# Kernel tuning notes

Measured on AMD Instinct MI355X. Metric: run time of the kernel, lower is better.

The kernel has to match this reference:

```python
import jax, jax.numpy as jnp
import numpy as np


def setup_inputs() -> dict:
    key = jax.random.key(0)
    k0, k1, k2, k3, k4 = jax.random.split(key, 5)
    T, B, S = 256, 8, 256          # tgt_len, batch, src_len
    QD, KD, VD = 512, 512, 512     # query_dim, key_dim, value_dim
    query = jax.random.normal(k0, (T, B, QD), dtype=jnp.float32)
    keys = jax.random.normal(k1, (B, S, KD), dtype=jnp.float32)
    values = jax.random.normal(k2, (B, S, VD), dtype=jnp.float32)
    # torch nn.Linear weights: (out_features, in_features)
    Wa = jax.random.normal(k3, (KD, QD + KD), dtype=jnp.float32) * 0.02
    va = jax.random.normal(k4, (1, KD), dtype=jnp.float32) * 0.02
    return {"query": query, "keys": keys, "values": values, "Wa": Wa, "va": va}


def reference(query, keys, values, Wa, va):
    # Wa(cat([q, k])) == q @ Wa[:, :QD].T + k @ Wa[:, QD:].T (algebraic split,
    # same math as the original concat, avoids materializing the concat tensor).
    QD = query.shape[-1]
    Wq, Wk = Wa[:, :QD], Wa[:, QD:]                      # (KD,QD), (KD,KD)
    qp = jnp.einsum('tbq,kq->btk', query, Wq)             # (B,T,KD)
    kp = jnp.einsum('bsk,hk->bsh', keys, Wk)              # (B,S,KD)
    hidden = jnp.tanh(qp[:, :, None, :] + kp[:, None, :, :])  # (B,T,S,KD)
    weight = jnp.einsum('btsk,k->bts', hidden, va[0])     # (B,T,S)
    score = jax.nn.softmax(weight, axis=-1)               # softmax over src
    ctx = jnp.einsum('bts,bsv->btv', score, values)       # (B,T,VD)
    return (score, ctx)
```

## Files before the change

### kernel.cpp

```cpp
#include <hip/hip_runtime.h>
#include <hip/hip_bf16.h>

#define TT   256
#define BB   8
#define SS   256
#define DD   512
#define C2LOG2E 2.8853900817779268f
#define LOG2E   1.4426950408889634f

typedef __attribute__((ext_vector_type(8))) short bf16x8;
typedef __attribute__((ext_vector_type(4))) float f32x4;

__device__ __forceinline__ unsigned short f2bf(float f) {
    unsigned u = __builtin_bit_cast(unsigned, f);
    u += 0x7FFFu + ((u >> 16) & 1u);
    return (unsigned short)(u >> 16);
}
__device__ __forceinline__ float bf2f(unsigned short h) {
    unsigned u = (unsigned)h << 16;
    return __builtin_bit_cast(float, u);
}

#define LDK 72
__global__ __launch_bounds__(256) void gemm_mfma(const float* __restrict__ query,
                                                 const float* __restrict__ keys,
                                                 const float* __restrict__ Wa,
                                                 float* __restrict__ eq,
                                                 float* __restrict__ ekT) {
    __shared__ __align__(16) unsigned char smem[4 * 64 * LDK * 2];
    unsigned short* sAh = (unsigned short*)smem;
    unsigned short* sAl = sAh + 64 * LDK;
    unsigned short* sBh = sAl + 64 * LDK;
    unsigned short* sBl = sBh + 64 * LDK;
    float* Cst = (float*)smem;

    const int idx = blockIdx.x;
    const int b   = idx & 7;
    const int r2  = idx >> 3;
    const int q   = r2 & 3;
    const int x   = (r2 >> 2) & 7;
    const int z   = r2 >> 5;
    const bool isQ = (z == 0);

    const float* A  = isQ ? query : keys;
    const int strideR = isQ ? BB * DD : DD;
    const int strideB = isQ ? DD : SS * DD;
    const float* Bsrc = Wa + (isQ ? 0 : DD);

    const int tileN = x * 64;

    const int tid = threadIdx.x;
    const int rb  = tid >> 4;
    const int c4  = tid & 15;

    const float* arow0 = A + (size_t)b * strideB + (size_t)(q * 64) * strideR;
    const float* brow0 = Bsrc + (size_t)tileN * (2 * DD);

    float4 av[4], bv[4];
    #pragma unroll
    for (int i = 0; i < 4; ++i) {
        av[i] = *(const float4*)(arow0 + (size_t)(rb + 16*i) * strideR + c4 * 4);
        bv[i] = *(const float4*)(brow0 + (size_t)(rb + 16*i) * (2*DD) + c4 * 4);
    }

    const int w    = tid >> 6;
    const int lane = tid & 63;
    const int wm   = (w >> 1) * 32;
    const int wn   = (w & 1) * 32;
    const int r16  = lane & 15;
    const int k8   = (lane >> 4) * 8;

    f32x4 acc[2][2] = {};

    for (int kb = 0; kb < DD; kb += 64) {
        __syncthreads();
        #pragma unroll
        for (int i = 0; i < 4; ++i) {
            const int row = rb + 16 * i;
            float4 a = av[i], bq = bv[i];
            ushort4 ah, al, bh, bl;
            ah.x = f2bf(a.x); al.x = f2bf(a.x - bf2f(ah.x));
            ah.y = f2bf(a.y); al.y = f2bf(a.y - bf2f(ah.y));
            ah.z = f2bf(a.z); al.z = f2bf(a.z - bf2f(ah.z));
            ah.w = f2bf(a.w); al.w = f2bf(a.w - bf2f(ah.w));
            bh.x = f2bf(bq.x); bl.x = f2bf(bq.x - bf2f(bh.x));
            bh.y = f2bf(bq.y); bl.y = f2bf(bq.y - bf2f(bh.y));
            bh.z = f2bf(bq.z); bl.z = f2bf(bq.z - bf2f(bh.z));
            bh.w = f2bf(bq.w); bl.w = f2bf(bq.w - bf2f(bh.w));
            *(ushort4*)(sAh + row * LDK + c4 * 4) = ah;
            *(ushort4*)(sAl + row * LDK + c4 * 4) = al;
            *(ushort4*)(sBh + row * LDK + c4 * 4) = bh;
            *(ushort4*)(sBl + row * LDK + c4 * 4) = bl;
        }
        __syncthreads();
        if (kb + 64 < DD) {
            #pragma unroll
            for (int i = 0; i < 4; ++i) {
                av[i] = *(const float4*)(arow0 + (size_t)(rb + 16*i) * strideR + kb + 64 + c4 * 4);
                bv[i] = *(const float4*)(brow0 + (size_t)(rb + 16*i) * (2*DD) + kb + 64 + c4 * 4);
            }
        }
        #pragma unroll
        for (int ks = 0; ks < 2; ++ks) {
            const int ko = ks * 32 + k8;
            bf16x8 a_h[2], a_l[2], b_h[2], b_l[2];
            #pragma unroll
            for (int mt = 0; mt < 2; ++mt) {
                a_h[mt] = *(const bf16x8*)(sAh + (wm + mt*16 + r16) * LDK + ko);
                a_l[mt] = *(const bf16x8*)(sAl + (wm + mt*16 + r16) * LDK + ko);
            }
            #pragma unroll
            for (int nt = 0; nt < 2; ++nt) {
                b_h[nt] = *(const bf16x8*)(sBh + (wn + nt*16 + r16) * LDK + ko);
                b_l[nt] = *(const bf16x8*)(sBl + (wn + nt*16 + r16) * LDK + ko);
            }
            #pragma unroll
            for (int mt = 0; mt < 2; ++mt)
                #pragma unroll
                for (int nt = 0; nt < 2; ++nt) {
                    acc[mt][nt] = __builtin_amdgcn_mfma_f32_16x16x32_bf16(a_h[mt], b_h[nt], acc[mt][nt], 0, 0, 0);
                    acc[mt][nt] = __builtin_amdgcn_mfma_f32_16x16x32_bf16(a_h[mt], b_l[nt], acc[mt][nt], 0, 0, 0);
                    acc[mt][nt] = __builtin_amdgcn_mfma_f32_16x16x32_bf16(a_l[mt], b_h[nt], acc[mt][nt], 0, 0, 0);
                }
        }
    }

    const int crow = (lane >> 4) * 4;
    if (isQ) {
        #pragma unroll
        for (int mt = 0; mt < 2; ++mt)
            #pragma unroll
            for (int nt = 0; nt < 2; ++nt)
                #pragma unroll
                for (int i = 0; i < 4; ++i) {
                    const int m = b * 256 + q * 64 + wm + mt*16 + crow + i;
                    const int n = tileN + wn + nt*16 + r16;
                    eq[(size_t)m * DD + n] = __builtin_amdgcn_exp2f(acc[mt][nt][i] * C2LOG2E);
                }
    } else {
        __syncthreads();
        #pragma unroll
        for (int mt = 0; mt < 2; ++mt)
            #pragma unroll
            for (int nt = 0; nt < 2; ++nt)
                #pragma unroll
                for (int i = 0; i < 4; ++i)
                    Cst[(wm + mt*16 + crow + i) * 69 + wn + nt*16 + r16] =
                        __builtin_amdgcn_exp2f(acc[mt][nt][i] * C2LOG2E);
        __syncthreads();
        const int n  = tid & 63;
        const int sg = tid >> 6;
        float* dst = ekT + (size_t)b * DD * SS + (size_t)(tileN + n) * SS + q * 64 + sg * 16;
        #pragma unroll
        for (int j4 = 0; j4 < 4; ++j4) {
            float4 o;
            o.x = Cst[(sg*16 + j4*4 + 0) * 69 + n];
            o.y = Cst[(sg*16 + j4*4 + 1) * 69 + n];
            o.z = Cst[(sg*16 + j4*4 + 2) * 69 + n];
            o.w = Cst[(sg*16 + j4*4 + 3) * 69 + n];
            *(float4*)(dst + j4 * 4) = o;
        }
    }
}

__global__ __launch_bounds__(1024, 8) void attn_fused(const float* __restrict__ eq,
                                                      const float* __restrict__ ekT,
                                                      const float* __restrict__ va,
                                                      const float* __restrict__ values,
                                                      float* __restrict__ out) {
    __shared__ __align__(16) float eq_s[4][512];
    __shared__ __align__(16) float vb_s[512];
    __shared__ __align__(16) float wacc[4][4][256];
    __shared__ __align__(16) float w_s[4][256];
    __shared__ float red_m[4][4];
    __shared__ float red_s[4][4];

    const int tid  = threadIdx.x;
    const int lane = tid & 63;
    const int w    = tid >> 6;
    const int kq   = w & 3;
    const int sq   = w >> 2;
    const int idx  = blockIdx.x;
    const int b    = idx & 7;
    const int t0   = (idx >> 3) * 4;

    if (tid < 512) {
        const float4* qsrc = (const float4*)(eq + (size_t)(b * TT + t0) * DD);
        ((float4*)&eq_s[0][0])[tid] = qsrc[tid];
    } else if (tid < 640) {
        const int i = tid - 512;
        float4 v = ((const float4*)va)[i];
        ((float4*)vb_s)[i] = make_float4(-2.f*v.x, -2.f*v.y, -2.f*v.z, -2.f*v.w);
    }
    __syncthreads();

    const int kbase = kq * 128;
    const int s     = sq * 64 + lane;
    const float* ekp = ekT + (size_t)b * DD * SS + (size_t)kbase * SS + s;
    const float4* eqr0 = (const float4*)&eq_s[0][kbase];
    const float4* eqr1 = (const float4*)&eq_s[1][kbase];
    const float4* eqr2 = (const float4*)&eq_s[2][kbase];
    const float4* eqr3 = (const float4*)&eq_s[3][kbase];
    const float4* vbr  = (const float4*)&vb_s[kbase];

    float acc0 = 0.f, acc1 = 0.f, acc2 = 0.f, acc3 = 0.f;

    #pragma unroll 4
    for (int kb = 0; kb < 128; kb += 4) {
        float ek0 = ekp[(size_t)(kb + 0) * SS];
        float ek1 = ekp[(size_t)(kb + 1) * SS];
        float ek2 = ekp[(size_t)(kb + 2) * SS];
        float ek3 = ekp[(size_t)(kb + 3) * SS];
        float4 e0 = eqr0[kb >> 2];
        float4 e1 = eqr1[kb >> 2];
        float4 e2 = eqr2[kb >> 2];
        float4 e3 = eqr3[kb >> 2];
        float4 vb = vbr[kb >> 2];
#define ASTEP(EC, EK, VC)                                                      \
        acc0 = fmaf(VC, __builtin_amdgcn_rcpf(fmaf(e0.EC, EK, 1.0f)), acc0);   \
        acc1 = fmaf(VC, __builtin_amdgcn_rcpf(fmaf(e1.EC, EK, 1.0f)), acc1);   \
        acc2 = fmaf(VC, __builtin_amdgcn_rcpf(fmaf(e2.EC, EK, 1.0f)), acc2);   \
        acc3 = fmaf(VC, __builtin_amdgcn_rcpf(fmaf(e3.EC, EK, 1.0f)), acc3);
        ASTEP(x, ek0, vb.x)
        ASTEP(y, ek1, vb.y)
        ASTEP(z, ek2, vb.z)
        ASTEP(w, ek3, vb.w)
#undef ASTEP
    }

    wacc[0][kq][s] = acc0;
    wacc[1][kq][s] = acc1;
    wacc[2][kq][s] = acc2;
    wacc[3][kq][s] = acc3;
    __syncthreads();

    float wt[4], p[4];
    if (kq == 0) {
        #pragma unroll
        for (int t = 0; t < 4; ++t)
            wt[t] = (wacc[t][0][s] + wacc[t][1][s]) + (wacc[t][2][s] + wacc[t][3][s]);
        #pragma unroll
        for (int t = 0; t < 4; ++t) {
            float m = wt[t];
            #pragma unroll
            for (int off = 32; off > 0; off >>= 1) m = fmaxf(m, __shfl_xor(m, off));
            if (lane == 0) red_m[sq][t] = m;
        }
    }
    __syncthreads();
    if (kq == 0) {
        #pragma unroll
        for (int t = 0; t < 4; ++t) {
            float M = fmaxf(fmaxf(red_m[0][t], red_m[1][t]),
                            fmaxf(red_m[2][t], red_m[3][t]));
            p[t] = __builtin_amdgcn_exp2f((wt[t] - M) * LOG2E);
            float sm = p[t];
            #pragma unroll
            for (int off = 32; off > 0; off >>= 1) sm += __shfl_xor(sm, off);
            if (lane == 0) red_s[sq][t] = sm;
        }
    }
    __syncthreads();
    if (kq == 0) {
        #pragma unroll
        for (int t = 0; t < 4; ++t) {
            float inv = __builtin_amdgcn_rcpf((red_s[0][t] + red_s[1][t]) +
                                              (red_s[2][t] + red_s[3][t]));
            float sc = p[t] * inv;
            out[(size_t)(b * TT + t0 + t) * SS + s] = sc;
            w_s[t][s] = sc;
        }
    }
    __syncthreads();

    const int v  = tid & 511;
    const int th = tid >> 9;
    const float* vcol = values + (size_t)b * SS * DD + v;
    const float4* wr0 = (const float4*)&w_s[th * 2][0];
    const float4* wr1 = (const float4*)&w_s[th * 2 + 1][0];
    float c0 = 0.f, c1 = 0.f;
    #pragma unroll 4
    for (int ss = 0; ss < SS; ss += 4) {
        float4 w0 = wr0[ss >> 2];
        float4 w1 = wr1[ss >> 2];
        float v0 = vcol[(size_t)(ss + 0) * DD];
        float v1 = vcol[(size_t)(ss + 1) * DD];
        float v2 = vcol[(size_t)(ss + 2) * DD];
        float v3 = vcol[(size_t)(ss + 3) * DD];
        c0 = fmaf(w0.x, v0, c0); c1 = fmaf(w1.x, v0, c1);
        c0 = fmaf(w0.y, v1, c0); c1 = fmaf(w1.y, v1, c1);
        c0 = fmaf(w0.z, v2, c0); c1 = fmaf(w1.z, v2, c1);
        c0 = fmaf(w0.w, v3, c0); c1 = fmaf(w1.w, v3, c1);
    }
    float* octx = out + (size_t)BB * TT * SS + (size_t)(b * TT + t0 + th * 2) * DD + v;
    octx[0]  = c0;
    octx[DD] = c1;
}

extern "C" void kernel_launch(void* const* d_in, const int* in_sizes, int n_in,
                              void* d_out, int out_size, void* d_ws, size_t ws_size,
                              hipStream_t stream) {
    const float* query  = (const float*)d_in[0];
    const float* keys   = (const float*)d_in[1];
    const float* values = (const float*)d_in[2];
    const float* Wa     = (const float*)d_in[3];
    const float* va     = (const float*)d_in[4];
    float* out = (float*)d_out;

    float* eq  = (float*)d_ws;
    float* ekT = eq + (size_t)BB * TT * DD;

    gemm_mfma<<<512, 256, 0, stream>>>(query, keys, Wa, eq, ekT);
    attn_fused<<<512, 1024, 0, stream>>>(eq, ekT, va, values, out);
}
```

Measured before the change: 71.05 us.

## Combine four reciprocals into one and store projected keys row-major

Groups of four terms v/(1+e_q*e_k) are now summed over a common denominator, so each group needs one rcp instead of four. Projected keys are written row-major, which drops the transpose through shared memory in the GEMM and lets the attention kernel read them with float4 loads. The softmax reduction now spreads its work across all four wave groups instead of only kq==0. The product of four denominators could overflow when the exponentials are large, and each lane's reads of ek are now strided across s rather than coalesced.

```diff
diff --git a/kernel.cpp b/kernel.cpp
--- a/kernel.cpp
+++ b/kernel.cpp
@@ -26,13 +26,12 @@
                                                  const float* __restrict__ keys,
                                                  const float* __restrict__ Wa,
                                                  float* __restrict__ eq,
-                                                 float* __restrict__ ekT) {
+                                                 float* __restrict__ ekR) {
     __shared__ __align__(16) unsigned char smem[4 * 64 * LDK * 2];
     unsigned short* sAh = (unsigned short*)smem;
     unsigned short* sAl = sAh + 64 * LDK;
     unsigned short* sBh = sAl + 64 * LDK;
     unsigned short* sBl = sBh + 64 * LDK;
-    float* Cst = (float*)smem;
 
     const int idx = blockIdx.x;
     const int b   = idx & 7;
@@ -46,9 +45,9 @@
     const int strideR = isQ ? BB * DD : DD;
     const int strideB = isQ ? DD : SS * DD;
     const float* Bsrc = Wa + (isQ ? 0 : DD);
+    float* dst = isQ ? eq : ekR;
 
     const int tileN = x * 64;
-
     const int tid = threadIdx.x;
     const int rb  = tid >> 4;
     const int c4  = tid & 15;
@@ -126,45 +125,20 @@
     }
 
     const int crow = (lane >> 4) * 4;
-    if (isQ) {
-        #pragma unroll
-        for (int mt = 0; mt < 2; ++mt)
-            #pragma unroll
-            for (int nt = 0; nt < 2; ++nt)
-                #pragma unroll
-                for (int i = 0; i < 4; ++i) {
-                    const int m = b * 256 + q * 64 + wm + mt*16 + crow + i;
-                    const int n = tileN + wn + nt*16 + r16;
-                    eq[(size_t)m * DD + n] = __builtin_amdgcn_exp2f(acc[mt][nt][i] * C2LOG2E);
-                }
-    } else {
-        __syncthreads();
-        #pragma unroll
-        for (int mt = 0; mt < 2; ++mt)
-            #pragma unroll
-            for (int nt = 0; nt < 2; ++nt)
-                #pragma unroll
-                for (int i = 0; i < 4; ++i)
-                    Cst[(wm + mt*16 + crow + i) * 69 + wn + nt*16 + r16] =
-                        __builtin_amdgcn_exp2f(acc[mt][nt][i] * C2LOG2E);
-        __syncthreads();
-        const int n  = tid & 63;
-        const int sg = tid >> 6;
-        float* dst = ekT + (size_t)b * DD * SS + (size_t)(tileN + n) * SS + q * 64 + sg * 16;
-        #pragma unroll
-        for (int j4 = 0; j4 < 4; ++j4) {
-            float4 o;
-            o.x = Cst[(sg*16 + j4*4 + 0) * 69 + n];
-            o.y = Cst[(sg*16 + j4*4 + 1) * 69 + n];
-            o.z = Cst[(sg*16 + j4*4 + 2) * 69 + n];
-            o.w = Cst[(sg*16 + j4*4 + 3) * 69 + n];
-            *(float4*)(dst + j4 * 4) = o;
-        }
-    }
+    #pragma unroll
+    for (int mt = 0; mt < 2; ++mt)
+        #pragma unroll
+        for (int nt = 0; nt < 2; ++nt)
+            #pragma unroll
+            for (int i = 0; i < 4; ++i) {
+                const int m = b * 256 + q * 64 + wm + mt*16 + crow + i;
+                const int n = tileN + wn + nt*16 + r16;
+                dst[(size_t)m * DD + n] = __builtin_amdgcn_exp2f(acc[mt][nt][i] * C2LOG2E);
+            }
 }
 
 __global__ __launch_bounds__(1024, 8) void attn_fused(const float* __restrict__ eq,
-                                                      const float* __restrict__ ekT,
+                                                      const float* __restrict__ ekR,
                                                       const float* __restrict__ va,
                                                       const float* __restrict__ values,
                                                       float* __restrict__ out) {
@@ -196,7 +170,7 @@
 
     const int kbase = kq * 128;
     const int s     = sq * 64 + lane;
-    const float* ekp = ekT + (size_t)b * DD * SS + (size_t)kbase * SS + s;
+    const float* ekp = ekR + (size_t)(b * SS + s) * DD + kbase;
     const float4* eqr0 = (const float4*)&eq_s[0][kbase];
     const float4* eqr1 = (const float4*)&eq_s[1][kbase];
     const float4* eqr2 = (const float4*)&eq_s[2][kbase];
@@ -207,25 +181,29 @@
 
     #pragma unroll 4
     for (int kb = 0; kb < 128; kb += 4) {
-        float ek0 = ekp[(size_t)(kb + 0) * SS];
-        float ek1 = ekp[(size_t)(kb + 1) * SS];
-        float ek2 = ekp[(size_t)(kb + 2) * SS];
-        float ek3 = ekp[(size_t)(kb + 3) * SS];
+        float4 ek = *(const float4*)(ekp + kb);
+        float4 vb = vbr[kb >> 2];
         float4 e0 = eqr0[kb >> 2];
         float4 e1 = eqr1[kb >> 2];
         float4 e2 = eqr2[kb >> 2];
         float4 e3 = eqr3[kb >> 2];
-        float4 vb = vbr[kb >> 2];
-#define ASTEP(EC, EK, VC)                                                      \
-        acc0 = fmaf(VC, __builtin_amdgcn_rcpf(fmaf(e0.EC, EK, 1.0f)), acc0);   \
-        acc1 = fmaf(VC, __builtin_amdgcn_rcpf(fmaf(e1.EC, EK, 1.0f)), acc1);   \
-        acc2 = fmaf(VC, __builtin_amdgcn_rcpf(fmaf(e2.EC, EK, 1.0f)), acc2);   \
-        acc3 = fmaf(VC, __builtin_amdgcn_rcpf(fmaf(e3.EC, EK, 1.0f)), acc3);
-        ASTEP(x, ek0, vb.x)
-        ASTEP(y, ek1, vb.y)
-        ASTEP(z, ek2, vb.z)
-        ASTEP(w, ek3, vb.w)
-#undef ASTEP
+#define GSTEP(EQ, ACC)                                                         \
+        {                                                                      \
+            float y0 = fmaf(EQ.x, ek.x, 1.0f);                                 \
+            float y1 = fmaf(EQ.y, ek.y, 1.0f);                                 \
+            float y2 = fmaf(EQ.z, ek.z, 1.0f);                                 \
+            float y3 = fmaf(EQ.w, ek.w, 1.0f);                                 \
+            float d01 = y0 * y1, d23 = y2 * y3;                                \
+            float n01 = fmaf(vb.x, y1, vb.y * y0);                             \
+            float n23 = fmaf(vb.z, y3, vb.w * y2);                             \
+            float num = fmaf(n01, d23, n23 * d01);                             \
+            ACC = fmaf(num, __builtin_amdgcn_rcpf(d01 * d23), ACC);            \
+        }
+        GSTEP(e0, acc0)
+        GSTEP(e1, acc1)
+        GSTEP(e2, acc2)
+        GSTEP(e3, acc3)
+#undef GSTEP
     }
 
     wacc[0][kq][s] = acc0;
@@ -234,42 +212,31 @@
     wacc[3][kq][s] = acc3;
     __syncthreads();
 
-    float wt[4], p[4];
-    if (kq == 0) {
-        #pragma unroll
-        for (int t = 0; t < 4; ++t)
-            wt[t] = (wacc[t][0][s] + wacc[t][1][s]) + (wacc[t][2][s] + wacc[t][3][s]);
-        #pragma unroll
-        for (int t = 0; t < 4; ++t) {
-            float m = wt[t];
-            #pragma unroll
-            for (int off = 32; off > 0; off >>= 1) m = fmaxf(m, __shfl_xor(m, off));
-            if (lane == 0) red_m[sq][t] = m;
-        }
-    }
-    __syncthreads();
-    if (kq == 0) {
-        #pragma unroll
-        for (int t = 0; t < 4; ++t) {
-            float M = fmaxf(fmaxf(red_m[0][t], red_m[1][t]),
-                            fmaxf(red_m[2][t], red_m[3][t]));
-            p[t] = __builtin_amdgcn_exp2f((wt[t] - M) * LOG2E);
-            float sm = p[t];
-            #pragma unroll
-            for (int off = 32; off > 0; off >>= 1) sm += __shfl_xor(sm, off);
-            if (lane == 0) red_s[sq][t] = sm;
-        }
-    }
-    __syncthreads();
-    if (kq == 0) {
-        #pragma unroll
-        for (int t = 0; t < 4; ++t) {
-            float inv = __builtin_amdgcn_rcpf((red_s[0][t] + red_s[1][t]) +
-                                              (red_s[2][t] + red_s[3][t]));
-            float sc = p[t] * inv;
-            out[(size_t)(b * TT + t0 + t) * SS + s] = sc;
-            w_s[t][s] = sc;
-        }
+    const int t = kq;
+    float wt = (wacc[t][0][s] + wacc[t][1][s]) + (wacc[t][2][s] + wacc[t][3][s]);
+    {
+        float m = wt;
+        #pragma unroll
+        for (int off = 32; off > 0; off >>= 1) m = fmaxf(m, __shfl_xor(m, off));
+        if (lane == 0) red_m[sq][t] = m;
+    }
+    __syncthreads();
+    float M = fmaxf(fmaxf(red_m[0][t], red_m[1][t]),
+                    fmaxf(red_m[2][t], red_m[3][t]));
+    float p = __builtin_amdgcn_exp2f((wt - M) * LOG2E);
+    {
+        float sm = p;
+        #pragma unroll
+        for (int off = 32; off > 0; off >>= 1) sm += __shfl_xor(sm, off);
+        if (lane == 0) red_s[sq][t] = sm;
+    }
+    __syncthreads();
+    {
+        float inv = __builtin_amdgcn_rcpf((red_s[0][t] + red_s[1][t]) +
+                                          (red_s[2][t] + red_s[3][t]));
+        float sc = p * inv;
+        out[(size_t)(b * TT + t0 + t) * SS + s] = sc;
+        w_s[t][s] = sc;
     }
     __syncthreads();
 
@@ -308,8 +275,8 @@
     float* out = (float*)d_out;
 
     float* eq  = (float*)d_ws;
-    float* ekT = eq + (size_t)BB * TT * DD;
-
-    gemm_mfma<<<512, 256, 0, stream>>>(query, keys, Wa, eq, ekT);
-    attn_fused<<<512, 1024, 0, stream>>>(eq, ekT, va, values, out);
-}
+    float* ekR = eq + (size_t)BB * TT * DD;
+
+    gemm_mfma<<<512, 256, 0, stream>>>(query, keys, Wa, eq, ekR);
+    attn_fused<<<512, 1024, 0, stream>>>(eq, ekR, va, values, out);
+}
```

Measured after the change: 72.45 us. About the same (+2.0%).

## Batch four reciprocals into one and restructure attention kernel thread mapping

Applied to the files above, without the earlier changes.

The attention kernel now sums four terms v_i/y_i over a common denominator, so it issues one rcp per four k-elements instead of four. Each thread also handles four source positions with float4 ekT loads over a 64-wide k slice, reads eq and va straight from global memory instead of LDS, and the block drops to 512 threads that each compute four context rows. The aim is to cut transcendental throughput cost and LDS traffic. In exchange it adds extra multiplies, risks overflow or precision loss in the product of four denominators, and leaves fewer threads per block.

```diff
diff --git a/kernel.cpp b/kernel.cpp
--- a/kernel.cpp
+++ b/kernel.cpp
@@ -48,7 +48,6 @@
     const float* Bsrc = Wa + (isQ ? 0 : DD);
 
     const int tileN = x * 64;
-
     const int tid = threadIdx.x;
     const int rb  = tid >> 4;
     const int c4  = tid & 15;
@@ -150,7 +149,7 @@
         __syncthreads();
         const int n  = tid & 63;
         const int sg = tid >> 6;
-        float* dst = ekT + (size_t)b * DD * SS + (size_t)(tileN + n) * SS + q * 64 + sg * 16;
+        float* dstp = ekT + (size_t)b * DD * SS + (size_t)(tileN + n) * SS + q * 64 + sg * 16;
         #pragma unroll
         for (int j4 = 0; j4 < 4; ++j4) {
             float4 o;
@@ -158,143 +157,152 @@
             o.y = Cst[(sg*16 + j4*4 + 1) * 69 + n];
             o.z = Cst[(sg*16 + j4*4 + 2) * 69 + n];
             o.w = Cst[(sg*16 + j4*4 + 3) * 69 + n];
-            *(float4*)(dst + j4 * 4) = o;
+            *(float4*)(dstp + j4 * 4) = o;
         }
     }
 }
 
-__global__ __launch_bounds__(1024, 8) void attn_fused(const float* __restrict__ eq,
-                                                      const float* __restrict__ ekT,
-                                                      const float* __restrict__ va,
-                                                      const float* __restrict__ values,
-                                                      float* __restrict__ out) {
-    __shared__ __align__(16) float eq_s[4][512];
-    __shared__ __align__(16) float vb_s[512];
-    __shared__ __align__(16) float wacc[4][4][256];
+__global__ __launch_bounds__(512, 4) void attn_fused(const float* __restrict__ eq,
+                                                     const float* __restrict__ ekT,
+                                                     const float* __restrict__ va,
+                                                     const float* __restrict__ values,
+                                                     float* __restrict__ out) {
+    __shared__ __align__(16) float wacc[8][4][256];
     __shared__ __align__(16) float w_s[4][256];
-    __shared__ float red_m[4][4];
-    __shared__ float red_s[4][4];
+    __shared__ float red_m[2][4];
+    __shared__ float red_s[2][4];
 
     const int tid  = threadIdx.x;
     const int lane = tid & 63;
     const int w    = tid >> 6;
-    const int kq   = w & 3;
-    const int sq   = w >> 2;
     const int idx  = blockIdx.x;
     const int b    = idx & 7;
     const int t0   = (idx >> 3) * 4;
-
-    if (tid < 512) {
-        const float4* qsrc = (const float4*)(eq + (size_t)(b * TT + t0) * DD);
-        ((float4*)&eq_s[0][0])[tid] = qsrc[tid];
-    } else if (tid < 640) {
-        const int i = tid - 512;
-        float4 v = ((const float4*)va)[i];
-        ((float4*)vb_s)[i] = make_float4(-2.f*v.x, -2.f*v.y, -2.f*v.z, -2.f*v.w);
-    }
+    const int k0   = w * 64;
+
+    const float* ekp = ekT + ((size_t)b * DD + k0) * SS + lane * 4;
+    const float4* qp0 = (const float4*)(eq + (size_t)(b * TT + t0 + 0) * DD + k0);
+    const float4* qp1 = (const float4*)(eq + (size_t)(b * TT + t0 + 1) * DD + k0);
+    const float4* qp2 = (const float4*)(eq + (size_t)(b * TT + t0 + 2) * DD + k0);
+    const float4* qp3 = (const float4*)(eq + (size_t)(b * TT + t0 + 3) * DD + k0);
+    const float4* vap = (const float4*)(va + k0);
+
+    float a00=0,a01=0,a02=0,a03=0, a10=0,a11=0,a12=0,a13=0;
+    float a20=0,a21=0,a22=0,a23=0, a30=0,a31=0,a32=0,a33=0;
+
+    #pragma unroll 4
+    for (int kb = 0; kb < 64; kb += 4) {
+        float4 ek0 = *(const float4*)(ekp + 0 * SS);
+        float4 ek1 = *(const float4*)(ekp + 1 * SS);
+        float4 ek2 = *(const float4*)(ekp + 2 * SS);
+        float4 ek3 = *(const float4*)(ekp + 3 * SS);
+        ekp += 4 * SS;
+        float4 q0 = qp0[kb >> 2];
+        float4 q1 = qp1[kb >> 2];
+        float4 q2 = qp2[kb >> 2];
+        float4 q3 = qp3[kb >> 2];
+        float4 v4 = vap[kb >> 2];
+#define GS(Q, E0, E1, E2, E3, ACC) {                                           \
+        float y0 = fmaf(Q.x, E0, 1.0f);                                        \
+        float y1 = fmaf(Q.y, E1, 1.0f);                                        \
+        float y2 = fmaf(Q.z, E2, 1.0f);                                        \
+        float y3 = fmaf(Q.w, E3, 1.0f);                                        \
+        float d01 = y0 * y1, d23 = y2 * y3;                                    \
+        float n01 = fmaf(v4.x, y1, v4.y * y0);                                 \
+        float n23 = fmaf(v4.z, y3, v4.w * y2);                                 \
+        ACC = fmaf(fmaf(n01, d23, n23 * d01),                                  \
+                   __builtin_amdgcn_rcpf(d01 * d23), ACC);                     \
+    }
+        GS(q0, ek0.x, ek1.x, ek2.x, ek3.x, a00)
+        GS(q0, ek0.y, ek1.y, ek2.y, ek3.y, a01)
+        GS(q0, ek0.z, ek1.z, ek2.z, ek3.z, a02)
+        GS(q0, ek0.w, ek1.w, ek2.w, ek3.w, a03)
+        GS(q1, ek0.x, ek1.x, ek2.x, ek3.x, a10)
+        GS(q1, ek0.y, ek1.y, ek2.y, ek3.y, a11)
+        GS(q1, ek0.z, ek1.z, ek2.z, ek3.z, a12)
+        GS(q1, ek0.w, ek1.w, ek2.w, ek3.w, a13)
+        GS(q2, ek0.x, ek1.x, ek2.x, ek3.x, a20)
+        GS(q2, ek0.y, ek1.y, ek2.y, ek3.y, a21)
+        GS(q2, ek0.z, ek1.z, ek2.z, ek3.z, a22)
+        GS(q2, ek0.w, ek1.w, ek2.w, ek3.w, a23)
+        GS(q3, ek0.x, ek1.x, ek2.x, ek3.x, a30)
+        GS(q3, ek0.y, ek1.y, ek2.y, ek3.y, a31)
+        GS(q3, ek0.z, ek1.z, ek2.z, ek3.z, a32)
+        GS(q3, ek0.w, ek1.w, ek2.w, ek3.w, a33)
+#undef GS
+    }
+
+    *(float4*)&wacc[w][0][lane * 4] = make_float4(a00, a01, a02, a03);
+    *(float4*)&wacc[w][1][lane * 4] = make_float4(a10, a11, a12, a13);
+    *(float4*)&wacc[w][2][lane * 4] = make_float4(a20, a21, a22, a23);
+    *(float4*)&wacc[w][3][lane * 4] = make_float4(a30, a31, a32, a33);
     __syncthreads();
 
-    const int kbase = kq * 128;
-    const int s     = sq * 64 + lane;
-    const float* ekp = ekT + (size_t)b * DD * SS + (size_t)kbase * SS + s;
-    const float4* eqr0 = (const float4*)&eq_s[0][kbase];
-    const float4* eqr1 = (const float4*)&eq_s[1][kbase];
-    const float4* eqr2 = (const float4*)&eq_s[2][kbase];
-    const float4* eqr3 = (const float4*)&eq_s[3][kbase];
-    const float4* vbr  = (const float4*)&vb_s[kbase];
-
-    float acc0 = 0.f, acc1 = 0.f, acc2 = 0.f, acc3 = 0.f;
-
+    const int t  = w & 3;
+    const int sh = w >> 2;
+    const int s1 = sh * 128 + lane;
+    const int s2 = s1 + 64;
+    float wt1 = 0.f, wt2 = 0.f;
+    #pragma unroll
+    for (int c = 0; c < 8; ++c) {
+        wt1 += wacc[c][t][s1];
+        wt2 += wacc[c][t][s2];
+    }
+    wt1 *= -2.0f; wt2 *= -2.0f;
+    {
+        float m = fmaxf(wt1, wt2);
+        #pragma unroll
+        for (int off = 32; off > 0; off >>= 1) m = fmaxf(m, __shfl_xor(m, off));
+        if (lane == 0) red_m[sh][t] = m;
+    }
+    __syncthreads();
+    const float M = fmaxf(red_m[0][t], red_m[1][t]);
+    float p1 = __builtin_amdgcn_exp2f((wt1 - M) * LOG2E);
+    float p2 = __builtin_amdgcn_exp2f((wt2 - M) * LOG2E);
+    {
+        float sm = p1 + p2;
+        #pragma unroll
+        for (int off = 32; off > 0; off >>= 1) sm += __shfl_xor(sm, off);
+        if (lane == 0) red_s[sh][t] = sm;
+    }
+    __syncthreads();
+    {
+        float inv = __builtin_amdgcn_rcpf(red_s[0][t] + red_s[1][t]);
+        float sc1 = p1 * inv, sc2 = p2 * inv;
+        float* orow = out + (size_t)(b * TT + t0 + t) * SS;
+        orow[s1] = sc1; orow[s2] = sc2;
+        w_s[t][s1] = sc1; w_s[t][s2] = sc2;
+    }
+    __syncthreads();
+
+    const float* vcol = values + (size_t)b * SS * DD + tid;
+    const float4* wr0 = (const float4*)&w_s[0][0];
+    const float4* wr1 = (const float4*)&w_s[1][0];
+    const float4* wr2 = (const float4*)&w_s[2][0];
+    const float4* wr3 = (const float4*)&w_s[3][0];
+    float c0 = 0.f, c1 = 0.f, c2 = 0.f, c3 = 0.f;
     #pragma unroll 4
-    for (int kb = 0; kb < 128; kb += 4) {
-        float ek0 = ekp[(size_t)(kb + 0) * SS];
-        float ek1 = ekp[(size_t)(kb + 1) * SS];
-        float ek2 = ekp[(size_t)(kb + 2) * SS];
-        float ek3 = ekp[(size_t)(kb + 3) * SS];
-        float4 e0 = eqr0[kb >> 2];
-        float4 e1 = eqr1[kb >> 2];
-        float4 e2 = eqr2[kb >> 2];
-        float4 e3 = eqr3[kb >> 2];
-        float4 vb = vbr[kb >> 2];
-#define ASTEP(EC, EK, VC)                                                      \
-        acc0 = fmaf(VC, __builtin_amdgcn_rcpf(fmaf(e0.EC, EK, 1.0f)), acc0);   \
-        acc1 = fmaf(VC, __builtin_amdgcn_rcpf(fmaf(e1.EC, EK, 1.0f)), acc1);   \
-        acc2 = fmaf(VC, __builtin_amdgcn_rcpf(fmaf(e2.EC, EK, 1.0f)), acc2);   \
-        acc3 = fmaf(VC, __builtin_amdgcn_rcpf(fmaf(e3.EC, EK, 1.0f)), acc3);
-        ASTEP(x, ek0, vb.x)
-        ASTEP(y, ek1, vb.y)
-        ASTEP(z, ek2, vb.z)
-        ASTEP(w, ek3, vb.w)
-#undef ASTEP
-    }
-
-    wacc[0][kq][s] = acc0;
-    wacc[1][kq][s] = acc1;
-    wacc[2][kq][s] = acc2;
-    wacc[3][kq][s] = acc3;
-    __syncthreads();
-
-    float wt[4], p[4];
-    if (kq == 0) {
-        #pragma unroll
-        for (int t = 0; t < 4; ++t)
-            wt[t] = (wacc[t][0][s] + wacc[t][1][s]) + (wacc[t][2][s] + wacc[t][3][s]);
-        #pragma unroll
-        for (int t = 0; t < 4; ++t) {
-            float m = wt[t];
-            #pragma unroll
-            for (int off = 32; off > 0; off >>= 1) m = fmaxf(m, __shfl_xor(m, off));
-            if (lane == 0) red_m[sq][t] = m;
-        }
-    }
-    __syncthreads();
-    if (kq == 0) {
-        #pragma unroll
-        for (int t = 0; t < 4; ++t) {
-            float M = fmaxf(fmaxf(red_m[0][t], red_m[1][t]),
-                            fmaxf(red_m[2][t], red_m[3][t]));
-            p[t] = __builtin_amdgcn_exp2f((wt[t] - M) * LOG2E);
-            float sm = p[t];
-            #pragma unroll
-            for (int off = 32; off > 0; off >>= 1) sm += __shfl_xor(sm, off);
-            if (lane == 0) red_s[sq][t] = sm;
-        }
-    }
-    __syncthreads();
-    if (kq == 0) {
-        #pragma unroll
-        for (int t = 0; t < 4; ++t) {
-            float inv = __builtin_amdgcn_rcpf((red_s[0][t] + red_s[1][t]) +
-                                              (red_s[2][t] + red_s[3][t]));
-            float sc = p[t] * inv;
-            out[(size_t)(b * TT + t0 + t) * SS + s] = sc;
-            w_s[t][s] = sc;
-        }
-    }
-    __syncthreads();
-
-    const int v  = tid & 511;
-    const int th = tid >> 9;
-    const float* vcol = values + (size_t)b * SS * DD + v;
-    const float4* wr0 = (const float4*)&w_s[th * 2][0];
-    const float4* wr1 = (const float4*)&w_s[th * 2 + 1][0];
-    float c0 = 0.f, c1 = 0.f;
-    #pragma unroll 4
-    for (int ss = 0; ss < SS; ss += 4) {
-        float4 w0 = wr0[ss >> 2];
-        float4 w1 = wr1[ss >> 2];
-        float v0 = vcol[(size_t)(ss + 0) * DD];
-        float v1 = vcol[(size_t)(ss + 1) * DD];
-        float v2 = vcol[(size_t)(ss + 2) * DD];
-        float v3 = vcol[(size_t)(ss + 3) * DD];
+    for (int s = 0; s < SS; s += 4) {
+        float4 w0 = wr0[s >> 2];
+        float4 w1 = wr1[s >> 2];
+        float4 w2 = wr2[s >> 2];
+        float4 w3 = wr3[s >> 2];
+        float v0 = vcol[(size_t)(s + 0) * DD];
+        float v1 = vcol[(size_t)(s + 1) * DD];
+        float v2 = vcol[(size_t)(s + 2) * DD];
+        float v3 = vcol[(size_t)(s + 3) * DD];
         c0 = fmaf(w0.x, v0, c0); c1 = fmaf(w1.x, v0, c1);
+        c2 = fmaf(w2.x, v0, c2); c3 = fmaf(w3.x, v0, c3);
         c0 = fmaf(w0.y, v1, c0); c1 = fmaf(w1.y, v1, c1);
+        c2 = fmaf(w2.y, v1, c2); c3 = fmaf(w3.y, v1, c3);
         c0 = fmaf(w0.z, v2, c0); c1 = fmaf(w1.z, v2, c1);
+        c2 = fmaf(w2.z, v2, c2); c3 = fmaf(w3.z, v2, c3);
         c0 = fmaf(w0.w, v3, c0); c1 = fmaf(w1.w, v3, c1);
-    }
-    float* octx = out + (size_t)BB * TT * SS + (size_t)(b * TT + t0 + th * 2) * DD + v;
-    octx[0]  = c0;
-    octx[DD] = c1;
+        c2 = fmaf(w2.w, v3, c2); c3 = fmaf(w3.w, v3, c3);
+    }
+    float* octx = out + (size_t)BB * TT * SS + (size_t)(b * TT + t0) * DD + tid;
+    octx[0 * DD] = c0; octx[1 * DD] = c1;
+    octx[2 * DD] = c2; octx[3 * DD] = c3;
 }
 
 extern "C" void kernel_launch(void* const* d_in, const int* in_sizes, int n_in,
@@ -311,5 +319,5 @@
     float* ekT = eq + (size_t)BB * TT * DD;
 
     gemm_mfma<<<512, 256, 0, stream>>>(query, keys, Wa, eq, ekT);
-    attn_fused<<<512, 1024, 0, stream>>>(eq, ekT, va, values, out);
-}
+    attn_fused<<<512, 512, 0, stream>>>(eq, ekT, va, values, out);
+}
```

After: 64.37 us. 1.1x faster.
